# Kernel optimization log

Measured on AMD Instinct MI355X. Metric: run time of the kernel, lower is better.

The kernel has to match this reference:

```python
import jax, jax.numpy as jnp
import numpy as np

EMBED_DIM = 384
NUM_HEADS = 6
HEAD_DIM = EMBED_DIM // NUM_HEADS
SCALE = HEAD_DIM ** (-0.5)
B, T, N = 8, 64, 196


def setup_inputs() -> dict:
    key = jax.random.key(0)
    k1, k2, k3, k4, k5 = jax.random.split(key, 5)
    x = jax.random.normal(k1, (B, T, N, EMBED_DIM), dtype=jnp.float32)
    W_qkv = jax.random.normal(k2, (3 * EMBED_DIM, EMBED_DIM), dtype=jnp.float32) * 0.02
    b_qkv = jax.random.normal(k3, (3 * EMBED_DIM,), dtype=jnp.float32) * 0.02
    W_proj = jax.random.normal(k4, (EMBED_DIM, EMBED_DIM), dtype=jnp.float32) * 0.02
    b_proj = jax.random.normal(k5, (EMBED_DIM,), dtype=jnp.float32) * 0.02
    return {"x": x, "W_qkv": W_qkv, "b_qkv": b_qkv, "W_proj": W_proj, "b_proj": b_proj}


def reference(x, W_qkv, b_qkv, W_proj, b_proj):
    b, t, n, c = x.shape
    # qkv projection: [B,T,N,3C] -> [B,T,N,3,H,hd] -> [3,B,H,T,N,hd]
    qkv = jnp.einsum('btnc,oc->btno', x, W_qkv) + b_qkv
    qkv = qkv.reshape(b, t, n, 3, NUM_HEADS, HEAD_DIM)
    qkv = jnp.transpose(qkv, (3, 0, 4, 1, 2, 5))
    q, k, v = qkv[0], qkv[1], qkv[2]
    q = q * SCALE
    # scores over patches within each block: [B,H,T,N,N]
    attn = jnp.einsum('bhtnd,bhtmd->bhtnm', q, k)
    attn = jax.nn.softmax(attn, axis=-1)
    out = jnp.einsum('bhtnm,bhtmd->bhtnd', attn, v)  # [B,H,T,N,hd]
    # Faithful to original: permute(0,2,3,4,1) puts head_dim before head, then flatten
    out = jnp.transpose(out, (0, 2, 3, 4, 1)).reshape(b, t, n, c)
    out = jnp.einsum('btnc,oc->btno', out, W_proj) + b_proj
    return out
```

## Files before the change

### kernel.cpp

```cpp
#include <hip/hip_runtime.h>
#include <cstdint>
#include <cstddef>

typedef unsigned short u16;
typedef __attribute__((ext_vector_type(4))) float f32x4;
typedef __attribute__((ext_vector_type(8))) __bf16 bf16x8;
typedef __attribute__((ext_vector_type(8))) unsigned short u16x8;
typedef __attribute__((ext_vector_type(4))) unsigned short u16x4;

#define M_TOTAL 100352
#define K_DIM   384
#define QKV_N   1152
#define NHEADS  6
#define NPAT    196
#define SCL     0.125f

__device__ __forceinline__ u16 f2bf(float f) {
    unsigned int u = __builtin_bit_cast(unsigned int, f);
    u += 0x7fffu + ((u >> 16) & 1u);
    return (u16)(u >> 16);
}

__device__ __forceinline__ void gload16(const void* g, void* l) {
    __builtin_amdgcn_global_load_lds(
        (const __attribute__((address_space(1))) unsigned int*)g,
        (__attribute__((address_space(3))) unsigned int*)l, 16, 0, 0);
}

__device__ __forceinline__ int xcd_swz(int bid, int per_xcd) {
    return (bid & 7) * per_xcd + (bid >> 3);
}

__global__ void cvt_bf16_kern(const float* __restrict__ in, u16* __restrict__ out, int n8) {
    int i = blockIdx.x * 256 + threadIdx.x;
    if (i >= n8) return;
    const float4* p = (const float4*)in + (size_t)i * 2;
    float4 a = p[0], b = p[1];
    u16x8 o;
    o[0]=f2bf(a.x); o[1]=f2bf(a.y); o[2]=f2bf(a.z); o[3]=f2bf(a.w);
    o[4]=f2bf(b.x); o[5]=f2bf(b.y); o[6]=f2bf(b.z); o[7]=f2bf(b.w);
    *((u16x8*)out + i) = o;
}

__global__ void cvt_wproj_kern(const float* __restrict__ in, u16* __restrict__ out) {
    int i = blockIdx.x * 256 + threadIdx.x;
    int o = i / 384;
    int c = i - o * 384;
    int d = c & 63, h = c >> 6;
    out[i] = f2bf(in[(size_t)o * 384 + d * 6 + h]);
}

template<int NOUT, bool BF16OUT, bool QSCALE>
__global__ __launch_bounds__(256, 2) void gemm_kern(
        const u16* __restrict__ A, const u16* __restrict__ Bw,
        const float* __restrict__ bias, void* __restrict__ outp) {
    constexpr int NB = NOUT / 128;
    constexpr int PER_XCD = (M_TOTAL / 128) * NB / 8;
    __shared__ u16 As[128 * 64];
    __shared__ u16 Bs[128 * 64];
    int wg = xcd_swz(blockIdx.x, PER_XCD);
    int bm = wg / NB, bn = wg % NB;
    int tid = threadIdx.x;
    int l = tid & 63, w = tid >> 6;
    int wr = w >> 1, wc = w & 1;
    f32x4 acc[4][4] = {};
    const u16* Ag = A + (size_t)bm * 128 * K_DIM;
    const u16* Bg = Bw + (size_t)bn * 128 * K_DIM;

    for (int ks = 0; ks < 6; ++ks) {
#pragma unroll
        for (int i = 0; i < 4; ++i) {
            int c = i * 256 + tid;
            int row = c >> 3, cc = c & 7;
            gload16(Ag + (size_t)row * K_DIM + ks * 64 + cc * 8, (u16*)As + c * 8);
            gload16(Bg + (size_t)row * K_DIM + ks * 64 + cc * 8, (u16*)Bs + c * 8);
        }
        __syncthreads();
#pragma unroll
        for (int kk = 0; kk < 2; ++kk) {
            bf16x8 af[4], bfr[4];
#pragma unroll
            for (int m = 0; m < 4; ++m)
                af[m] = *(const bf16x8*)&As[(wr * 64 + m * 16 + (l & 15)) * 64 + kk * 32 + (l >> 4) * 8];
#pragma unroll
            for (int n = 0; n < 4; ++n)
                bfr[n] = *(const bf16x8*)&Bs[(wc * 64 + n * 16 + (l & 15)) * 64 + kk * 32 + (l >> 4) * 8];
#pragma unroll
            for (int m = 0; m < 4; ++m)
#pragma unroll
                for (int n = 0; n < 4; ++n)
                    acc[m][n] = __builtin_amdgcn_mfma_f32_16x16x32_bf16(af[m], bfr[n], acc[m][n], 0, 0, 0);
        }
        __syncthreads();
    }
#pragma unroll
    for (int n = 0; n < 4; ++n) {
        int col = bn * 128 + wc * 64 + n * 16 + (l & 15);
        float bv = bias[col];
#pragma unroll
        for (int m = 0; m < 4; ++m) {
            int row0 = bm * 128 + wr * 64 + m * 16 + (l >> 4) * 4;
#pragma unroll
            for (int r = 0; r < 4; ++r) {
                float v = acc[m][n][r] + bv;
                if constexpr (QSCALE) { if (col < 384) v *= SCL; }
                if constexpr (BF16OUT)
                    ((u16*)outp)[(size_t)(row0 + r) * NOUT + col] = f2bf(v);
                else
                    ((float*)outp)[(size_t)(row0 + r) * NOUT + col] = v;
            }
        }
    }
}

__global__ __launch_bounds__(256, 2) void attn_kern(const u16* __restrict__ qkv,
                                                    u16* __restrict__ osc) {
    __shared__ u16 k_lds[208 * 72];
    __shared__ u16 vT[64 * 232];
    __shared__ u16 p_lds[4 * 16 * 36];

    int wg = xcd_swz(blockIdx.x, 384);
    int h = wg % NHEADS;
    int bt = wg / NHEADS;
    size_t m_base = (size_t)bt * NPAT;
    int tid = threadIdx.x, l = tid & 63, w = tid >> 6;

    {
        int d0 = (tid & 7) * 8;
#pragma unroll
        for (int it = 0; it < 7; ++it) {
            int n = it * 32 + (tid >> 3);
            if (n < 208) {
                u16x8 val = {};
                if (n < 196)
                    val = *(const u16x8*)(qkv + (m_base + n) * QKV_N + 384 + h * 64 + d0);
                *(u16x8*)&k_lds[n * 72 + d0] = val;
            }
        }
    }
    {
        int d0 = w * 16;
#pragma unroll
        for (int it = 0; it < 4; ++it) {
            int n = it * 64 + l;
            if (n < 232) {
                u16x8 v0 = {}, v1 = {};
                if (n < 196) {
                    const u16* src = qkv + (m_base + n) * QKV_N + 768 + h * 64 + d0;
                    v0 = *(const u16x8*)src;
                    v1 = *(const u16x8*)(src + 8);
                }
#pragma unroll
                for (int j = 0; j < 8; ++j) {
                    vT[(d0 + j) * 232 + n] = v0[j];
                    vT[(d0 + 8 + j) * 232 + n] = v1[j];
                }
            }
        }
    }
    __syncthreads();

    u16* pw = &p_lds[w * 16 * 36];
    for (int qt = w; qt < 13; qt += 4) {
        int q0 = qt * 16;
        int qrow = q0 + (l & 15); if (qrow > 195) qrow = 195;
        const u16* qsrc = qkv + (m_base + qrow) * QKV_N + h * 64 + (l >> 4) * 8;
        bf16x8 aq0 = *(const bf16x8*)qsrc;
        bf16x8 aq1 = *(const bf16x8*)(qsrc + 32);

        f32x4 s[13];
#pragma unroll
        for (int f = 0; f < 13; ++f) {
            f32x4 a = {};
            bf16x8 b0 = *(const bf16x8*)&k_lds[(f * 16 + (l & 15)) * 72 + (l >> 4) * 8];
            a = __builtin_amdgcn_mfma_f32_16x16x32_bf16(aq0, b0, a, 0, 0, 0);
            bf16x8 b1 = *(const bf16x8*)&k_lds[(f * 16 + (l & 15)) * 72 + 32 + (l >> 4) * 8];
            a = __builtin_amdgcn_mfma_f32_16x16x32_bf16(aq1, b1, a, 0, 0, 0);
            s[f] = a;
        }
        float rs[4] = {0.f, 0.f, 0.f, 0.f};
#pragma unroll
        for (int f = 0; f < 13; ++f) {
#pragma unroll
            for (int r = 0; r < 4; ++r) {
                float e = __expf(s[f][r]);
                if (f == 12 && (l & 15) >= 4) e = 0.f;
                s[f][r] = e;
                rs[r] += e;
            }
        }
#pragma unroll
        for (int r = 0; r < 4; ++r) {
            float t = rs[r];
            t += __shfl_xor(t, 1);
            t += __shfl_xor(t, 2);
            t += __shfl_xor(t, 4);
            t += __shfl_xor(t, 8);
            rs[r] = __builtin_amdgcn_rcpf(t);
        }
        f32x4 o[4] = {};
#pragma unroll
        for (int kb = 0; kb < 7; ++kb) {
#pragma unroll
            for (int fh = 0; fh < 2; ++fh) {
                int f = kb * 2 + fh;
#pragma unroll
                for (int r = 0; r < 4; ++r) {
                    float pv = 0.f;
                    if (f < 13) pv = s[f][r];
                    pw[((l >> 4) * 4 + r) * 36 + fh * 16 + (l & 15)] = f2bf(pv);
                }
            }
            u16x4 lo = *(const u16x4*)&pw[(l & 15) * 36 + (l >> 4) * 8];
            u16x4 hi = *(const u16x4*)&pw[(l & 15) * 36 + (l >> 4) * 8 + 4];
            union { u16x4 h4[2]; bf16x8 v8; } uu;
            uu.h4[0] = lo; uu.h4[1] = hi;
            bf16x8 pa = uu.v8;
#pragma unroll
            for (int j = 0; j < 4; ++j) {
                bf16x8 bv = *(const bf16x8*)&vT[(j * 16 + (l & 15)) * 232 + kb * 32 + (l >> 4) * 8];
                o[j] = __builtin_amdgcn_mfma_f32_16x16x32_bf16(pa, bv, o[j], 0, 0, 0);
            }
        }
#pragma unroll
        for (int j = 0; j < 4; ++j) {
#pragma unroll
            for (int r = 0; r < 4; ++r) {
                int q = q0 + (l >> 4) * 4 + r;
                if (q < 196)
                    osc[(m_base + q) * 384 + h * 64 + j * 16 + (l & 15)] = f2bf(o[j][r] * rs[r]);
            }
        }
    }
}

extern "C" void kernel_launch(void* const* d_in, const int* in_sizes, int n_in,
                              void* d_out, int out_size, void* d_ws, size_t ws_size,
                              hipStream_t stream) {
    const float* x     = (const float*)d_in[0];
    const float* Wqkv  = (const float*)d_in[1];
    const float* bqkv  = (const float*)d_in[2];
    const float* Wproj = (const float*)d_in[3];
    const float* bproj = (const float*)d_in[4];

    const size_t need = ((size_t)M_TOTAL * 384 + (size_t)M_TOTAL * QKV_N
                         + (size_t)QKV_N * K_DIM + (size_t)K_DIM * K_DIM) * 2;
    if (ws_size < need) {
        hipMemsetAsync(d_out, 0, (size_t)out_size * 4, stream);
        return;
    }

    u16* xbf    = (u16*)d_ws;
    u16* qkvb   = xbf + (size_t)M_TOTAL * 384;
    u16* wqkvb  = qkvb + (size_t)M_TOTAL * QKV_N;
    u16* wprojb = wqkvb + (size_t)QKV_N * K_DIM;

    cvt_bf16_kern<<<18816, 256, 0, stream>>>(x, xbf, 4816896);
    cvt_bf16_kern<<<216, 256, 0, stream>>>(Wqkv, wqkvb, 55296);
    cvt_wproj_kern<<<576, 256, 0, stream>>>(Wproj, wprojb);

    gemm_kern<QKV_N, true, true><<<7056, 256, 0, stream>>>(xbf, wqkvb, bqkv, qkvb);
    attn_kern<<<3072, 256, 0, stream>>>(qkvb, xbf);
    gemm_kern<384, false, false><<<2352, 256, 0, stream>>>(xbf, wprojb, bproj, (float*)d_out);
}
```

Measured before the change: 358.2 us.

## Fuse x fp32-to-bf16 conversion into register-resident A-tile GEMM

Drops the separate pass that converts x to bf16 and instead has the QKV GEMM load fp32 rows and convert them in registers. The GEMM is restructured so each wave keeps a full 16x384 A row-slab in registers and streams B fragments straight from global memory (no LDS), looping over 128-column output chunks, with occupancy hint raised to 3. This removes one full read/write pass over x and the LDS staging, at the cost of uncoalesced, repeated B loads from global/L2 and higher register pressure.

```diff
diff --git a/kernel.cpp b/kernel.cpp
--- a/kernel.cpp
+++ b/kernel.cpp
@@ -19,12 +19,6 @@
     unsigned int u = __builtin_bit_cast(unsigned int, f);
     u += 0x7fffu + ((u >> 16) & 1u);
     return (u16)(u >> 16);
-}
-
-__device__ __forceinline__ void gload16(const void* g, void* l) {
-    __builtin_amdgcn_global_load_lds(
-        (const __attribute__((address_space(1))) unsigned int*)g,
-        (__attribute__((address_space(3))) unsigned int*)l, 16, 0, 0);
 }
 
 __device__ __forceinline__ int xcd_swz(int bid, int per_xcd) {
@@ -50,64 +44,61 @@
     out[i] = f2bf(in[(size_t)o * 384 + d * 6 + h]);
 }
 
-template<int NOUT, bool BF16OUT, bool QSCALE>
-__global__ __launch_bounds__(256, 2) void gemm_kern(
-        const u16* __restrict__ A, const u16* __restrict__ Bw,
+template<int NOUT, bool BF16OUT, bool QSCALE, bool AF32>
+__global__ __launch_bounds__(256, 3) void gemm_kern(
+        const void* __restrict__ Ap, const u16* __restrict__ Bw,
         const float* __restrict__ bias, void* __restrict__ outp) {
-    constexpr int NB = NOUT / 128;
-    constexpr int PER_XCD = (M_TOTAL / 128) * NB / 8;
-    __shared__ u16 As[128 * 64];
-    __shared__ u16 Bs[128 * 64];
+    constexpr int NCH = NOUT / 128;
+    constexpr int PER_XCD = (M_TOTAL / 64) / 8;
     int wg = xcd_swz(blockIdx.x, PER_XCD);
-    int bm = wg / NB, bn = wg % NB;
-    int tid = threadIdx.x;
-    int l = tid & 63, w = tid >> 6;
-    int wr = w >> 1, wc = w & 1;
-    f32x4 acc[4][4] = {};
-    const u16* Ag = A + (size_t)bm * 128 * K_DIM;
-    const u16* Bg = Bw + (size_t)bn * 128 * K_DIM;
-
-    for (int ks = 0; ks < 6; ++ks) {
-#pragma unroll
-        for (int i = 0; i < 4; ++i) {
-            int c = i * 256 + tid;
-            int row = c >> 3, cc = c & 7;
-            gload16(Ag + (size_t)row * K_DIM + ks * 64 + cc * 8, (u16*)As + c * 8);
-            gload16(Bg + (size_t)row * K_DIM + ks * 64 + cc * 8, (u16*)Bs + c * 8);
-        }
-        __syncthreads();
-#pragma unroll
-        for (int kk = 0; kk < 2; ++kk) {
-            bf16x8 af[4], bfr[4];
-#pragma unroll
-            for (int m = 0; m < 4; ++m)
-                af[m] = *(const bf16x8*)&As[(wr * 64 + m * 16 + (l & 15)) * 64 + kk * 32 + (l >> 4) * 8];
-#pragma unroll
-            for (int n = 0; n < 4; ++n)
-                bfr[n] = *(const bf16x8*)&Bs[(wc * 64 + n * 16 + (l & 15)) * 64 + kk * 32 + (l >> 4) * 8];
-#pragma unroll
-            for (int m = 0; m < 4; ++m)
-#pragma unroll
-                for (int n = 0; n < 4; ++n)
-                    acc[m][n] = __builtin_amdgcn_mfma_f32_16x16x32_bf16(af[m], bfr[n], acc[m][n], 0, 0, 0);
-        }
-        __syncthreads();
-    }
-#pragma unroll
-    for (int n = 0; n < 4; ++n) {
-        int col = bn * 128 + wc * 64 + n * 16 + (l & 15);
-        float bv = bias[col];
-#pragma unroll
-        for (int m = 0; m < 4; ++m) {
-            int row0 = bm * 128 + wr * 64 + m * 16 + (l >> 4) * 4;
+    int tid = threadIdx.x, l = tid & 63, w = tid >> 6;
+    size_t row0 = (size_t)wg * 64 + w * 16;
+    int lr = l & 15, lg = l >> 4;
+
+    bf16x8 af[12];
+    if constexpr (AF32) {
+        const float* ar = (const float*)Ap + (row0 + lr) * K_DIM + lg * 8;
+#pragma unroll
+        for (int kk = 0; kk < 12; ++kk) {
+            f32x4 lo = *(const f32x4*)(ar + kk * 32);
+            f32x4 hi = *(const f32x4*)(ar + kk * 32 + 4);
+            bf16x8 t;
+            t[0]=(__bf16)lo[0]; t[1]=(__bf16)lo[1]; t[2]=(__bf16)lo[2]; t[3]=(__bf16)lo[3];
+            t[4]=(__bf16)hi[0]; t[5]=(__bf16)hi[1]; t[6]=(__bf16)hi[2]; t[7]=(__bf16)hi[3];
+            af[kk] = t;
+        }
+    } else {
+        const u16* ar = (const u16*)Ap + (row0 + lr) * K_DIM + lg * 8;
+#pragma unroll
+        for (int kk = 0; kk < 12; ++kk)
+            af[kk] = *(const bf16x8*)(ar + kk * 32);
+    }
+
+    for (int ch = 0; ch < NCH; ++ch) {
+        int nbase = ch * 128;
+        const u16* br = Bw + (size_t)(nbase + lr) * K_DIM + lg * 8;
+        f32x4 acc[8] = {};
+#pragma unroll
+        for (int kk = 0; kk < 12; ++kk) {
+#pragma unroll
+            for (int nf = 0; nf < 8; ++nf) {
+                bf16x8 b = *(const bf16x8*)(br + (size_t)nf * 16 * K_DIM + kk * 32);
+                acc[nf] = __builtin_amdgcn_mfma_f32_16x16x32_bf16(af[kk], b, acc[nf], 0, 0, 0);
+            }
+        }
+#pragma unroll
+        for (int nf = 0; nf < 8; ++nf) {
+            int col = nbase + nf * 16 + lr;
+            float bv = bias[col];
 #pragma unroll
             for (int r = 0; r < 4; ++r) {
-                float v = acc[m][n][r] + bv;
+                size_t row = row0 + lg * 4 + r;
+                float v = acc[nf][r] + bv;
                 if constexpr (QSCALE) { if (col < 384) v *= SCL; }
                 if constexpr (BF16OUT)
-                    ((u16*)outp)[(size_t)(row0 + r) * NOUT + col] = f2bf(v);
+                    ((u16*)outp)[row * NOUT + col] = f2bf(v);
                 else
-                    ((float*)outp)[(size_t)(row0 + r) * NOUT + col] = v;
+                    ((float*)outp)[row * NOUT + col] = v;
             }
         }
     }
@@ -250,16 +241,15 @@
         return;
     }
 
-    u16* xbf    = (u16*)d_ws;
-    u16* qkvb   = xbf + (size_t)M_TOTAL * 384;
+    u16* obf    = (u16*)d_ws;
+    u16* qkvb   = obf + (size_t)M_TOTAL * 384;
     u16* wqkvb  = qkvb + (size_t)M_TOTAL * QKV_N;
     u16* wprojb = wqkvb + (size_t)QKV_N * K_DIM;
 
-    cvt_bf16_kern<<<18816, 256, 0, stream>>>(x, xbf, 4816896);
     cvt_bf16_kern<<<216, 256, 0, stream>>>(Wqkv, wqkvb, 55296);
     cvt_wproj_kern<<<576, 256, 0, stream>>>(Wproj, wprojb);
 
-    gemm_kern<QKV_N, true, true><<<7056, 256, 0, stream>>>(xbf, wqkvb, bqkv, qkvb);
-    attn_kern<<<3072, 256, 0, stream>>>(qkvb, xbf);
-    gemm_kern<384, false, false><<<2352, 256, 0, stream>>>(xbf, wprojb, bproj, (float*)d_out);
-}
+    gemm_kern<QKV_N, true, true, true><<<1568, 256, 0, stream>>>(x, wqkvb, bqkv, qkvb);
+    attn_kern<<<3072, 256, 0, stream>>>(qkvb, obf);
+    gemm_kern<384, false, false, false><<<1568, 256, 0, stream>>>(obf, wprojb, bproj, (float*)d_out);
+}
```

Measured after the change: 1.090 ms. 3.04x slower.
